# Kernel tuning notes

Measured on AMD Instinct MI355X. Metric: run time of the kernel, lower is better.

Reference implementation:

```python
import jax, jax.numpy as jnp
import numpy as np

EMBED = 384
HEAD = 64


def setup_inputs() -> dict:
    key = jax.random.key(0)
    kx, kq, kk, kv = jax.random.split(key, 4)
    B, T = 4, 4096
    x = jax.random.normal(kx, (B, T, EMBED), dtype=jnp.float32)
    # torch Linear(384, 64, bias=False): weight (64, 384), y = x @ W.T.
    # Store pre-transposed as (EMBED, HEAD) so y = x @ W.
    s = 1.0 / np.sqrt(EMBED)  # kaiming-uniform-ish scale
    Wq = jax.random.uniform(kq, (EMBED, HEAD), jnp.float32, -s, s)
    Wk = jax.random.uniform(kk, (EMBED, HEAD), jnp.float32, -s, s)
    Wv = jax.random.uniform(kv, (EMBED, HEAD), jnp.float32, -s, s)
    return {"x": x, "Wq": Wq, "Wk": Wk, "Wv": Wv}


def reference(x, Wq, Wk, Wv):
    # q, k, v: [B, T, H]
    q = x @ Wq
    k = x @ Wk
    v = x @ Wv
    scale = k.shape[-1] ** (-0.5)
    scores = jnp.einsum("bth,bsh->bts", q, k) * scale  # [B, T, T]
    # Faithful to the original: tril, then mask anything equal to 0 with -inf
    # (this also masks exact zeros inside the causal region).
    tril = jnp.tril(scores)
    masked = jnp.where(tril == 0, -jnp.inf, tril)
    attn = jax.nn.softmax(masked, axis=-1)
    out = jnp.einsum("bts,bsh->bth", attn, v)  # [B, T, H]
    return out
```

## Files before the change

kernel.cpp:

```cpp
#include <hip/hip_runtime.h>
#include <hip/hip_bf16.h>
#include <stdint.h>


#define EMBED 384
#define HEAD  64
#define NB    4
#define NT    4096
#define NROWS (NB * NT)
#define NSPLIT 4

#define SCALE_Q 0.18033688011112042f

typedef short bf16x8 __attribute__((ext_vector_type(8)));
typedef float f32x4  __attribute__((ext_vector_type(4)));
typedef float f32x16 __attribute__((ext_vector_type(16)));

__device__ __forceinline__ unsigned short bfround(float f) {
    union { float f; unsigned u; } v; v.f = f;
    return (unsigned short)((v.u + 0x8000u) >> 16);
}
__device__ __forceinline__ unsigned packbf(float lo, float hi) {
    union { float f; unsigned u; } a, b; a.f = lo; b.f = hi;
    return ((a.u + 0x8000u) >> 16) | ((b.u + 0x8000u) & 0xFFFF0000u);
}
__device__ __forceinline__ unsigned cvtpk(float lo, float hi) {
    unsigned r;
    asm("v_cvt_pk_bf16_f32 %0, %1, %2" : "=v"(r) : "v"(lo), "v"(hi));
    return r;
}
__device__ __forceinline__ void pl_swap32(unsigned& a, unsigned& b) {
    asm("v_permlane32_swap_b32 %0, %1" : "+v"(a), "+v"(b));
}

__global__ __launch_bounds__(256)
void wprep_kernel(const float* __restrict__ Wq,
                  const float* __restrict__ Wk,
                  const float* __restrict__ Wv,
                  unsigned short* __restrict__ Wt)
{
    int idx = blockIdx.x * 256 + threadIdx.x;
    int k = idx / 192;
    int n = idx - k * 192;
    int sel = n >> 6, nc = n & 63;
    const float* wp = (sel == 0) ? Wq : ((sel == 1) ? Wk : Wv);
    Wt[n * EMBED + k] = bfround(wp[(size_t)k * HEAD + nc]);
}

__global__ __launch_bounds__(512)
void proj_kernel(const float* __restrict__ x,
                 const unsigned short* __restrict__ Wt,
                 unsigned short* __restrict__ Qo,
                 unsigned short* __restrict__ Ko,
                 unsigned short* __restrict__ Vto)
{
    __shared__ __attribute__((aligned(16))) unsigned short ws[2][192][128];
    __shared__ __attribute__((aligned(16))) unsigned short xs[2][64][128];
    unsigned short (*vbuf)[72] = (unsigned short (*)[72])&xs[1][0][0];

    const int t    = threadIdx.x;
    const int lane = t & 63;
    const int w    = t >> 6;
    const int quad = lane >> 4;
    const int l16  = lane & 15;
    const int wr   = w & 3;
    const int wc   = w >> 2;
    const int r0   = blockIdx.x * 64;

    const int xr  = t >> 5, xc4 = t & 31;
    const int xch = xc4 >> 1, xsub = (xc4 & 1) * 4;
    const int wrw = t >> 4, wcc = t & 15;

    f32x4 acc[6];
#pragma unroll
    for (int i = 0; i < 6; ++i) acc[i] = (f32x4){0.f, 0.f, 0.f, 0.f};

    float4 xv[4];
    uint4  wv[6];
#pragma unroll
    for (int i = 0; i < 4; ++i)
        xv[i] = *(const float4*)(x + (size_t)(r0 + xr + 16 * i) * EMBED + xc4 * 4);
#pragma unroll
    for (int i = 0; i < 6; ++i)
        wv[i] = *(const uint4*)(Wt + (size_t)(wrw + 32 * i) * EMBED + wcc * 8);

    int cur = 0;
#pragma unroll
    for (int ph = 0; ph < 3; ++ph) {
#pragma unroll
        for (int i = 0; i < 4; ++i) {
            int row = xr + 16 * i;
            uint2 pw; pw.x = packbf(xv[i].x, xv[i].y); pw.y = packbf(xv[i].z, xv[i].w);
            *(uint2*)&xs[cur][row][((xch ^ (row & 15)) << 3) + xsub] = pw;
        }
#pragma unroll
        for (int i = 0; i < 6; ++i) {
            int row = wrw + 32 * i;
            *(uint4*)&ws[cur][row][(wcc ^ (row & 15)) << 3] = wv[i];
        }
        __syncthreads();

        if (ph < 2) {
            const int k0 = (ph + 1) * 128;
#pragma unroll
            for (int i = 0; i < 4; ++i)
                xv[i] = *(const float4*)(x + (size_t)(r0 + xr + 16 * i) * EMBED + k0 + xc4 * 4);
#pragma unroll
            for (int i = 0; i < 6; ++i)
                wv[i] = *(const uint4*)(Wt + (size_t)(wrw + 32 * i) * EMBED + k0 + wcc * 8);
        }

#pragma unroll
        for (int s = 0; s < 4; ++s) {
            bf16x8 a = *(const bf16x8*)&xs[cur][wr * 16 + l16][((s * 4 + quad) ^ l16) << 3];
#pragma unroll
            for (int ng = 0; ng < 6; ++ng) {
                bf16x8 b = *(const bf16x8*)&ws[cur][wc * 96 + ng * 16 + l16][((s * 4 + quad) ^ l16) << 3];
                acc[ng] = __builtin_amdgcn_mfma_f32_16x16x32_bf16(a, b, acc[ng], 0, 0, 0);
            }
        }
        cur ^= 1;
    }
    __syncthreads();

#pragma unroll
    for (int ng = 0; ng < 6; ++ng) {
        int cg = wc * 96 + ng * 16 + l16;
#pragma unroll
        for (int r = 0; r < 4; ++r) {
            int row = r0 + wr * 16 + quad * 4 + r;
            float vv = acc[ng][r];
            if (cg < 64) {
                Qo[(size_t)row * HEAD + cg] = bfround(vv * SCALE_Q);
            } else if (cg < 128) {
                Ko[(size_t)row * HEAD + (cg - 64)] = bfround(vv);
            } else {
                vbuf[cg - 128][wr * 16 + quad * 4 + r] = bfround(vv);
            }
        }
    }
    __syncthreads();
    {
        const int batch = r0 >> 12;
        const int s0 = r0 & (NT - 1);
        const int d = t >> 3, c = t & 7;
        *(uint4*)(Vto + ((size_t)(batch * HEAD + d)) * NT + s0 + c * 8) =
            *(const uint4*)&vbuf[d][c * 8];
    }
}

__global__ __launch_bounds__(256, 4)
void attn_kernel(const unsigned short* __restrict__ Qi,
                 const unsigned short* __restrict__ Ki,
                 const unsigned short* __restrict__ Vti,
                 float* __restrict__ opart,
                 float* __restrict__ lpart)
{
    __shared__ __attribute__((aligned(16))) unsigned short KV[2][2][64][64];
    __shared__ float rsc[64];

    const int t    = threadIdx.x;
    const int w    = t >> 6;
    const int lane = t & 63;
    const int l32  = lane & 31;
    const int hi   = lane >> 5;
    const int qg   = w >> 1;
    const int sh   = w & 1;

    const int u = blockIdx.x;
    const int g = u >> 4;
    const int m = (g < 32) ? (63 - g) : (g - 32);
    const int sp = (u >> 2) & 3;
    const int batch = u & 3;
    const int ntiles = (m >= sp) ? (((m - sp) >> 2) + 1) : 0;
    const int q0w = m * 64 + qg * 32;

    const unsigned short* Kbg = Ki  + (size_t)batch * NT * HEAD;
    const unsigned short* Vbg = Vti + (size_t)batch * HEAD * NT;

    bf16x8 bq[4];
#pragma unroll
    for (int dc = 0; dc < 4; ++dc)
        bq[dc] = *(const bf16x8*)(Qi + (size_t)(batch * NT + q0w + l32) * HEAD
                                  + dc * 16 + hi * 8);

    f32x16 o0, o1;
#pragma unroll
    for (int i = 0; i < 16; ++i) { o0[i] = 0.f; o1[i] = 0.f; }
    float rs = 0.f;

    const int srow0 = t >> 3, sc = t & 7;
    const int srow1 = srow0 + 32;
    const int scc0 = sc ^ (srow0 & 7);
    const int scc1 = sc ^ (srow1 & 7);
    const int r7 = l32 & 7;

    uint4 kr0, kr1, vr0, vr1;
    if (ntiles > 0) {
        kr0 = *(const uint4*)(Kbg + (size_t)(sp * 64 + srow0) * HEAD + sc * 8);
        kr1 = *(const uint4*)(Kbg + (size_t)(sp * 64 + srow1) * HEAD + sc * 8);
        vr0 = *(const uint4*)(Vbg + (size_t)srow0 * NT + sp * 64 + sc * 8);
        vr1 = *(const uint4*)(Vbg + (size_t)srow1 * NT + sp * 64 + sc * 8);
    }

    int cur = 0;
    for (int j = 0; j < ntiles; ++j) {
        const int kt = sp + 4 * j;
        *(uint4*)&KV[cur][0][srow0][scc0 * 8] = kr0;
        *(uint4*)&KV[cur][0][srow1][scc1 * 8] = kr1;
        *(uint4*)&KV[cur][1][srow0][scc0 * 8] = vr0;
        *(uint4*)&KV[cur][1][srow1][scc1 * 8] = vr1;
        __syncthreads();

        if (j + 1 < ntiles) {
            const int ktn = kt + 4;
            kr0 = *(const uint4*)(Kbg + (size_t)(ktn * 64 + srow0) * HEAD + sc * 8);
            kr1 = *(const uint4*)(Kbg + (size_t)(ktn * 64 + srow1) * HEAD + sc * 8);
            vr0 = *(const uint4*)(Vbg + (size_t)srow0 * NT + ktn * 64 + sc * 8);
            vr1 = *(const uint4*)(Vbg + (size_t)srow1 * NT + ktn * 64 + sc * 8);
        }

        f32x16 z;
#pragma unroll
        for (int i = 0; i < 16; ++i) z[i] = 0.f;
        const unsigned short* kb = &KV[cur][0][sh * 32 + l32][0];
#pragma unroll
        for (int dc = 0; dc < 4; ++dc) {
            bf16x8 ak = *(const bf16x8*)&kb[(((dc << 1) | hi) ^ r7) << 3];
            z = __builtin_amdgcn_mfma_f32_32x32x16_bf16(ak, bq[dc], z, 0, 0, 0);
        }

        const bool diag = (kt == m);
        const int qglob = q0w + l32;
        float pq[16];
#pragma unroll
        for (int r = 0; r < 16; ++r) {
            float pv = __builtin_amdgcn_exp2f(z[r]);
            if (diag) {
                int sg = kt * 64 + sh * 32 + (r & 3) + 8 * (r >> 2) + 4 * hi;
                pv = (sg > qglob) ? 0.f : pv;
            }
            pq[r] = pv;
        }
        rs += (((pq[0] + pq[1]) + (pq[2] + pq[3])) + ((pq[4] + pq[5]) + (pq[6] + pq[7])))
            + (((pq[8] + pq[9]) + (pq[10] + pq[11])) + ((pq[12] + pq[13]) + (pq[14] + pq[15])));

        unsigned x0 = cvtpk(pq[0], pq[1]),  x1 = cvtpk(pq[2], pq[3]);
        unsigned x2 = cvtpk(pq[4], pq[5]),  x3 = cvtpk(pq[6], pq[7]);
        unsigned x4 = cvtpk(pq[8], pq[9]),  x5 = cvtpk(pq[10], pq[11]);
        unsigned x6 = cvtpk(pq[12], pq[13]), x7 = cvtpk(pq[14], pq[15]);
        pl_swap32(x0, x2); pl_swap32(x1, x3);
        pl_swap32(x4, x6); pl_swap32(x5, x7);
        union { unsigned uu[4]; bf16x8 v; } b0, b1;
        b0.uu[0] = x0; b0.uu[1] = x1; b0.uu[2] = x2; b0.uu[3] = x3;
        b1.uu[0] = x4; b1.uu[1] = x5; b1.uu[2] = x6; b1.uu[3] = x7;

        const unsigned short* vb0 = &KV[cur][1][l32][0];
        const unsigned short* vb1 = &KV[cur][1][32 + l32][0];
#pragma unroll
        for (int sk = 0; sk < 2; ++sk) {
            const int c = sh * 4 + sk * 2 + hi;
            bf16x8 av0 = *(const bf16x8*)&vb0[((c ^ r7) << 3)];
            bf16x8 av1 = *(const bf16x8*)&vb1[((c ^ r7) << 3)];
            const bf16x8 bp = sk ? b1.v : b0.v;
            o0 = __builtin_amdgcn_mfma_f32_32x32x16_bf16(av0, bp, o0, 0, 0, 0);
            o1 = __builtin_amdgcn_mfma_f32_32x32x16_bf16(av1, bp, o1, 0, 0, 0);
        }
        cur ^= 1;
    }

    float rs2 = rs + __shfl_xor(rs, 32, 64);
    __syncthreads();
    float (*osc)[65] = (float (*)[65])&KV[0][0][0][0];
    if (sh == 1) {
#pragma unroll
        for (int r = 0; r < 16; ++r) {
            osc[(r & 3) + 8 * (r >> 2) + 4 * hi][qg * 32 + l32] = o0[r];
            osc[32 + (r & 3) + 8 * (r >> 2) + 4 * hi][qg * 32 + l32] = o1[r];
        }
        if (lane < 32) rsc[qg * 32 + l32] = rs2;
    }
    __syncthreads();
    if (sh == 0) {
#pragma unroll
        for (int r = 0; r < 16; ++r) {
            osc[(r & 3) + 8 * (r >> 2) + 4 * hi][qg * 32 + l32] += o0[r];
            osc[32 + (r & 3) + 8 * (r >> 2) + 4 * hi][qg * 32 + l32] += o1[r];
        }
        if (lane < 32) {
            float rtot = rs2 + rsc[qg * 32 + l32];
            lpart[(size_t)sp * NROWS + batch * NT + m * 64 + qg * 32 + l32] = rtot;
        }
    }
    __syncthreads();
    {
        float* ob = opart + (size_t)sp * NROWS * HEAD
                  + (size_t)(batch * NT + m * 64) * HEAD;
        const int d0 = (t & 15) * 4;
#pragma unroll
        for (int i = 0; i < 4; ++i) {
            const int q = i * 16 + (t >> 4);
            f32x4 v;
            v[0] = osc[d0 + 0][q]; v[1] = osc[d0 + 1][q];
            v[2] = osc[d0 + 2][q]; v[3] = osc[d0 + 3][q];
            *(f32x4*)&ob[(size_t)q * HEAD + d0] = v;
        }
    }
}

__global__ __launch_bounds__(256)
void combine_kernel(const float* __restrict__ opart,
                    const float* __restrict__ lpart,
                    float* __restrict__ out)
{
    int gid = blockIdx.x * 256 + threadIdx.x;
    int row = gid >> 4;
    int d4  = (gid & 15) * 4;
    const size_t st = (size_t)NROWS * HEAD;
    const float* p0 = opart + (size_t)row * HEAD + d4;
    f32x4 a = *(const f32x4*)(p0);
    f32x4 b = *(const f32x4*)(p0 + st);
    f32x4 c = *(const f32x4*)(p0 + 2 * st);
    f32x4 d = *(const f32x4*)(p0 + 3 * st);
    float inv = 1.0f / (lpart[row] + lpart[NROWS + row] +
                        lpart[2 * NROWS + row] + lpart[3 * NROWS + row]);
    f32x4 res = (a + b) + (c + d);
    res[0] *= inv; res[1] *= inv; res[2] *= inv; res[3] *= inv;
    *(f32x4*)(out + (size_t)row * HEAD + d4) = res;
}

extern "C" void kernel_launch(void* const* d_in, const int* in_sizes, int n_in,
                              void* d_out, int out_size, void* d_ws, size_t ws_size,
                              hipStream_t stream)
{
    const float* x  = (const float*)d_in[0];
    const float* Wq = (const float*)d_in[1];
    const float* Wk = (const float*)d_in[2];
    const float* Wv = (const float*)d_in[3];
    float* out = (float*)d_out;

    unsigned short* Qw  = (unsigned short*)d_ws;
    unsigned short* Kw  = Qw + (size_t)NROWS * HEAD;
    unsigned short* Vtw = Kw + (size_t)NROWS * HEAD;
    unsigned short* Wtw = Vtw + (size_t)NROWS * HEAD;
    float* opart = (float*)(Wtw + (size_t)192 * EMBED);
    float* lpart = opart + (size_t)NSPLIT * NROWS * HEAD;

    wprep_kernel<<<(192 * EMBED) / 256, 256, 0, stream>>>(Wq, Wk, Wv, Wtw);
    proj_kernel<<<256, 512, 0, stream>>>(x, Wtw, Qw, Kw, Vtw);
    attn_kernel<<<1024, 256, 0, stream>>>(Qw, Kw, Vtw, opart, lpart);
    combine_kernel<<<NROWS * 16 / 256, 256, 0, stream>>>(opart, lpart, out);
}
```

Measured before the change: 104.8 us.

## Give each wave private K/V LDS slices and drop per-tile block barrier

Each wave now loads only the 32 K rows and 32 V columns it consumes into its own LDS region, so the per-tile __syncthreads and double buffering are removed. Both query-group waves sharing a key half now load the same K/V data separately, which doubles global-to-LDS traffic. The V tile uses a padded, narrower row stride with its own XOR swizzle. The occupancy hint of 4 blocks per CU is also dropped.

```diff
diff --git a/kernel.cpp b/kernel.cpp
--- a/kernel.cpp
+++ b/kernel.cpp
@@ -149,14 +149,14 @@
     }
 }
 
-__global__ __launch_bounds__(256, 4)
+__global__ __launch_bounds__(256)
 void attn_kernel(const unsigned short* __restrict__ Qi,
                  const unsigned short* __restrict__ Ki,
                  const unsigned short* __restrict__ Vti,
                  float* __restrict__ opart,
                  float* __restrict__ lpart)
 {
-    __shared__ __attribute__((aligned(16))) unsigned short KV[2][2][64][64];
+    __shared__ __attribute__((aligned(16))) unsigned short smem[17408];
     __shared__ float rsc[64];
 
     const int t    = threadIdx.x;
@@ -175,6 +175,9 @@
     const int ntiles = (m >= sp) ? (((m - sp) >> 2) + 1) : 0;
     const int q0w = m * 64 + qg * 32;
 
+    unsigned short* Kw = smem + w * 2048;
+    unsigned short* Vw = smem + 8192 + w * 2304;
+
     const unsigned short* Kbg = Ki  + (size_t)batch * NT * HEAD;
     const unsigned short* Vbg = Vti + (size_t)batch * HEAD * NT;
 
@@ -189,41 +192,42 @@
     for (int i = 0; i < 16; ++i) { o0[i] = 0.f; o1[i] = 0.f; }
     float rs = 0.f;
 
-    const int srow0 = t >> 3, sc = t & 7;
-    const int srow1 = srow0 + 32;
-    const int scc0 = sc ^ (srow0 & 7);
-    const int scc1 = sc ^ (srow1 & 7);
+    const int krow = lane >> 3, kc = lane & 7;
+    const int vrow = lane >> 2, vc = lane & 3;
     const int r7 = l32 & 7;
-
-    uint4 kr0, kr1, vr0, vr1;
+    const int r3 = l32 & 3;
+
+    uint4 kr[4], vr[4];
     if (ntiles > 0) {
-        kr0 = *(const uint4*)(Kbg + (size_t)(sp * 64 + srow0) * HEAD + sc * 8);
-        kr1 = *(const uint4*)(Kbg + (size_t)(sp * 64 + srow1) * HEAD + sc * 8);
-        vr0 = *(const uint4*)(Vbg + (size_t)srow0 * NT + sp * 64 + sc * 8);
-        vr1 = *(const uint4*)(Vbg + (size_t)srow1 * NT + sp * 64 + sc * 8);
-    }
-
-    int cur = 0;
+#pragma unroll
+        for (int i = 0; i < 4; ++i) {
+            kr[i] = *(const uint4*)(Kbg + (size_t)(sp * 64 + sh * 32 + krow + 8 * i) * HEAD + kc * 8);
+            vr[i] = *(const uint4*)(Vbg + (size_t)(vrow + 16 * i) * NT + sp * 64 + sh * 32 + vc * 8);
+        }
+    }
+
     for (int j = 0; j < ntiles; ++j) {
         const int kt = sp + 4 * j;
-        *(uint4*)&KV[cur][0][srow0][scc0 * 8] = kr0;
-        *(uint4*)&KV[cur][0][srow1][scc1 * 8] = kr1;
-        *(uint4*)&KV[cur][1][srow0][scc0 * 8] = vr0;
-        *(uint4*)&KV[cur][1][srow1][scc1 * 8] = vr1;
-        __syncthreads();
-
+#pragma unroll
+        for (int i = 0; i < 4; ++i) {
+            const int r = krow + 8 * i;
+            *(uint4*)&Kw[r * 64 + ((kc ^ (r & 7)) << 3)] = kr[i];
+            const int d = vrow + 16 * i;
+            *(uint4*)&Vw[d * 36 + ((vc ^ (d & 3)) << 3)] = vr[i];
+        }
         if (j + 1 < ntiles) {
             const int ktn = kt + 4;
-            kr0 = *(const uint4*)(Kbg + (size_t)(ktn * 64 + srow0) * HEAD + sc * 8);
-            kr1 = *(const uint4*)(Kbg + (size_t)(ktn * 64 + srow1) * HEAD + sc * 8);
-            vr0 = *(const uint4*)(Vbg + (size_t)srow0 * NT + ktn * 64 + sc * 8);
-            vr1 = *(const uint4*)(Vbg + (size_t)srow1 * NT + ktn * 64 + sc * 8);
+#pragma unroll
+            for (int i = 0; i < 4; ++i) {
+                kr[i] = *(const uint4*)(Kbg + (size_t)(ktn * 64 + sh * 32 + krow + 8 * i) * HEAD + kc * 8);
+                vr[i] = *(const uint4*)(Vbg + (size_t)(vrow + 16 * i) * NT + ktn * 64 + sh * 32 + vc * 8);
+            }
         }
 
         f32x16 z;
 #pragma unroll
         for (int i = 0; i < 16; ++i) z[i] = 0.f;
-        const unsigned short* kb = &KV[cur][0][sh * 32 + l32][0];
+        const unsigned short* kb = &Kw[l32 * 64];
 #pragma unroll
         for (int dc = 0; dc < 4; ++dc) {
             bf16x8 ak = *(const bf16x8*)&kb[(((dc << 1) | hi) ^ r7) << 3];
@@ -255,23 +259,22 @@
         b0.uu[0] = x0; b0.uu[1] = x1; b0.uu[2] = x2; b0.uu[3] = x3;
         b1.uu[0] = x4; b1.uu[1] = x5; b1.uu[2] = x6; b1.uu[3] = x7;
 
-        const unsigned short* vb0 = &KV[cur][1][l32][0];
-        const unsigned short* vb1 = &KV[cur][1][32 + l32][0];
+        const unsigned short* vb0 = &Vw[l32 * 36];
+        const unsigned short* vb1 = &Vw[(32 + l32) * 36];
 #pragma unroll
         for (int sk = 0; sk < 2; ++sk) {
-            const int c = sh * 4 + sk * 2 + hi;
-            bf16x8 av0 = *(const bf16x8*)&vb0[((c ^ r7) << 3)];
-            bf16x8 av1 = *(const bf16x8*)&vb1[((c ^ r7) << 3)];
+            const int cc = sk * 2 + hi;
+            bf16x8 av0 = *(const bf16x8*)&vb0[((cc ^ r3) << 3)];
+            bf16x8 av1 = *(const bf16x8*)&vb1[((cc ^ r3) << 3)];
             const bf16x8 bp = sk ? b1.v : b0.v;
             o0 = __builtin_amdgcn_mfma_f32_32x32x16_bf16(av0, bp, o0, 0, 0, 0);
             o1 = __builtin_amdgcn_mfma_f32_32x32x16_bf16(av1, bp, o1, 0, 0, 0);
         }
-        cur ^= 1;
     }
 
     float rs2 = rs + __shfl_xor(rs, 32, 64);
     __syncthreads();
-    float (*osc)[65] = (float (*)[65])&KV[0][0][0][0];
+    float (*osc)[65] = (float (*)[65])&smem[0];
     if (sh == 1) {
 #pragma unroll
         for (int r = 0; r < 16; ++r) {
```

New measurement: 173.2 us. 1.65x slower.
